# Kernel optimization log

Hardware: AMD Instinct MI355X
Metric: run time of the kernel (lower is better)

## Reference

```python
import jax, jax.numpy as jnp
import numpy as np

B, S, C = 16, 4096, 512
T_MAX = 512          # static max target length (padded, masked)
BETA = 1.0
CIF_EPS = 1e-4
LN_EPS = 1e-5
EXTRA_STEPS = 2      # max number of extra full fires per timestep (alpha<=1 after scaling => rarely >0)


def setup_inputs() -> dict:
    key = jax.random.key(0)
    ks = jax.random.split(key, 5)
    return {
        "x": jax.random.normal(ks[0], (B, S, C), jnp.float32),
        "encoder_padding_mask": jnp.zeros((B, S), bool),
        "target_lengths": jax.random.randint(ks[1], (B,), 1, T_MAX + 1),
        "conv_w": jax.random.normal(ks[2], (C, C, 3), jnp.float32) * 0.02,  # (out,in,k) torch layout
        "conv_b": jnp.zeros((C,), jnp.float32),
        "ln_g": jnp.ones((C,), jnp.float32),
        "ln_b": jnp.zeros((C,), jnp.float32),
        "proj_w": jax.random.normal(ks[3], (C, 1), jnp.float32) * (1.0 / np.sqrt(C)),
        "proj_b": jnp.zeros((1,), jnp.float32),
    }


def weight_predictor(x, conv_w, conv_b, ln_g, ln_b, proj_w, proj_b):
    # x: (B,S,C) -> alpha: (B,S) in (0,1). Dropout is eval-mode identity.
    h = jnp.transpose(x, (0, 2, 1))  # (B,C,S)
    h = jax.lax.conv_general_dilated(
        h, conv_w, window_strides=(1,), padding='SAME',
        dimension_numbers=('NCH', 'OIH', 'NCH')) + conv_b[None, :, None]
    h = jnp.transpose(h, (0, 2, 1))  # (B,S,C)
    mu = jnp.mean(h, -1, keepdims=True)
    var = jnp.mean((h - mu) ** 2, -1, keepdims=True)
    h = (h - mu) * jax.lax.rsqrt(var + LN_EPS) * ln_g + ln_b
    h = jax.nn.gelu(h, approximate=False)
    return jax.nn.sigmoid(h @ proj_w + proj_b)[..., 0]  # (B,S)


def cif(x, alpha, target_lengths):
    # torch-cif parallel formulation (training branch with target_lengths scaling)
    Bb, Ss, Cc = x.shape
    alpha_sum = jnp.sum(alpha, 1)                                   # (B,)
    desired = BETA * target_lengths.astype(alpha.dtype) + CIF_EPS
    alpha = alpha * (desired / alpha_sum)[:, None]
    csum = jnp.cumsum(alpha, 1)                                     # (B,S)
    right_idx = jnp.minimum(jnp.floor(csum / BETA).astype(jnp.int32), T_MAX)
    left_idx = jnp.concatenate(
        [jnp.zeros((Bb, 1), jnp.int32), right_idx[:, :-1]], axis=1)
    fire_num = right_idx - left_idx
    extra = jnp.maximum(fire_num - 1, 0)
    right_w = jnp.where(fire_num > 0, csum - right_idx.astype(alpha.dtype) * BETA, 0.0)
    left_w = alpha - right_w - extra.astype(alpha.dtype) * BETA

    bidx = jnp.arange(Bb)[:, None]  # (B,1) broadcast over S
    out = jnp.zeros((Bb, T_MAX + 1, Cc), x.dtype)
    out = out.at[bidx, left_idx].add(left_w[..., None] * x)
    out = out.at[bidx, right_idx].add(right_w[..., None] * x)
    # extra full-beta fires for steps whose alpha crosses multiple thresholds
    tgt = left_idx
    ew = extra
    for _ in range(EXTRA_STEPS):
        tgt = jnp.minimum(tgt + 1, T_MAX)
        m = (ew > 0).astype(x.dtype)
        out = out.at[bidx, tgt].add((BETA * m)[..., None] * x)
        ew = ew - 1
    out = out[:, :T_MAX]
    valid = (jnp.arange(T_MAX)[None, :] < target_lengths[:, None])  # (B,T)
    return out * valid[..., None]


def reference(x, encoder_padding_mask, target_lengths,
              conv_w, conv_b, ln_g, ln_b, proj_w, proj_b):
    # weight_predictor_stop_gradient=True: detach x for alpha
    alpha = weight_predictor(jax.lax.stop_gradient(x),
                             conv_w, conv_b, ln_g, ln_b, proj_w, proj_b)
    pad = encoder_padding_mask
    x = jnp.where(pad[..., None], 0.0, x)
    alpha = jnp.where(pad, 0.0, alpha)
    return cif(x, alpha, target_lengths)  # (B, T_MAX, C)
```

## Files before the change

### kernel.cpp

```cpp
#include <hip/hip_runtime.h>
#include <math.h>

#define B_DIM 16
#define S_LEN 4096
#define C_DIM 512
#define TMAXI 512

typedef __attribute__((ext_vector_type(8))) short bfrag;
typedef __attribute__((ext_vector_type(4))) float facc;

__device__ __forceinline__ unsigned short f2bf(float f) {
  unsigned u = __float_as_uint(f);
  unsigned r = u + 0x7FFFu + ((u >> 16) & 1u);
  return (unsigned short)(r >> 16);
}
__device__ __forceinline__ float bf2f(unsigned short h) {
  return __uint_as_float(((unsigned)h) << 16);
}

__device__ __forceinline__ void gload16(const void* g, void* l) {
  __builtin_amdgcn_global_load_lds(
      (const __attribute__((address_space(1))) unsigned int*)g,
      (__attribute__((address_space(3))) unsigned int*)l, 16, 0, 0);
}

__device__ __forceinline__ float wave_reduce_add(float v) {
#pragma unroll
  for (int off = 32; off > 0; off >>= 1) v += __shfl_xor(v, off, 64);
  return v;
}

__global__ __launch_bounds__(256) void k_split_x(const float* __restrict__ x,
                                                 unsigned short* __restrict__ xph,
                                                 unsigned short* __restrict__ xpl) {
  const size_t total = (size_t)B_DIM * (S_LEN + 2) * C_DIM;
  size_t e0 = ((size_t)blockIdx.x * 256 + threadIdx.x) * 8;
  if (e0 >= total) return;
  int b = (int)(e0 / ((size_t)(S_LEN + 2) * C_DIM));
  size_t r = e0 - (size_t)b * (S_LEN + 2) * C_DIM;
  int sp = (int)(r / C_DIM);
  int c = (int)(r % C_DIM);
  unsigned short hv[8], lv[8];
  if (sp == 0 || sp == S_LEN + 1) {
#pragma unroll
    for (int j = 0; j < 8; ++j) { hv[j] = 0; lv[j] = 0; }
  } else {
    const float* xs = &x[((size_t)b * S_LEN + (sp - 1)) * C_DIM + c];
    float4 v0 = *(const float4*)xs;
    float4 v1 = *(const float4*)(xs + 4);
    float vv[8] = {v0.x, v0.y, v0.z, v0.w, v1.x, v1.y, v1.z, v1.w};
#pragma unroll
    for (int j = 0; j < 8; ++j) {
      unsigned short h = f2bf(vv[j]);
      hv[j] = h;
      lv[j] = f2bf(vv[j] - bf2f(h));
    }
  }
  *(uint4*)&xph[e0] = *(const uint4*)hv;
  *(uint4*)&xpl[e0] = *(const uint4*)lv;
}

__global__ __launch_bounds__(256) void k_split_w(const float* __restrict__ w,
                                                 unsigned short* __restrict__ wh,
                                                 unsigned short* __restrict__ wl) {
  int idx = blockIdx.x * 256 + threadIdx.x;
  if (idx >= C_DIM * C_DIM) return;
  const float* src = &w[(size_t)idx * 3];
#pragma unroll
  for (int dk = 0; dk < 3; ++dk) {
    float v = src[dk];
    unsigned short h = f2bf(v);
    wh[(size_t)dk * (C_DIM * C_DIM) + idx] = h;
    wl[(size_t)dk * (C_DIM * C_DIM) + idx] = f2bf(v - bf2f(h));
  }
}

__global__ __launch_bounds__(512) void k_fused(const unsigned short* __restrict__ xph,
                                               const unsigned short* __restrict__ xpl,
                                               const unsigned short* __restrict__ wh,
                                               const unsigned short* __restrict__ wl,
                                               const float* __restrict__ conv_b,
                                               const float* __restrict__ ln_g,
                                               const float* __restrict__ ln_b,
                                               const float* __restrict__ pw,
                                               const float* __restrict__ pb,
                                               const unsigned char* __restrict__ mask,
                                               float* __restrict__ alpha) {
  __shared__ short At[64 * 64];
  __shared__ short Bt[512 * 64];

  const int t = threadIdx.x;
  const int lane = t & 63;
  const int wid = t >> 6;
  const int wr = wid >> 2;
  const int wc = wid & 3;
  const int lr = lane & 15;
  const int kg = lane >> 4;

  const int m0 = blockIdx.x * 64;
  const int b = m0 >> 12;
  const int s0 = m0 & (S_LEN - 1);

  const int arow = t >> 3;
  const int aps = t & 7;
  const int als = aps ^ (arow & 7);
  const unsigned short* asrc_base =
      (als < 4 ? xph : xpl) + ((size_t)b * (S_LEN + 2) + (s0 + arow)) * C_DIM + (als & 3) * 8;

  const unsigned short* bsrc_base[8];
#pragma unroll
  for (int r = 0; r < 8; ++r) {
    int c = r * 512 + t;
    int row = c >> 3;
    int ls = (c & 7) ^ (row & 7);
    bsrc_base[r] = (ls < 4 ? wh : wl) + (size_t)row * C_DIM + (ls & 3) * 8;
  }

  facc acc[2][8];
#pragma unroll
  for (int fm = 0; fm < 2; ++fm)
#pragma unroll
    for (int fn = 0; fn < 8; ++fn) acc[fm][fn] = (facc)0.f;

  for (int q = 0; q < 48; ++q) {
    const int dk = q >> 4;
    const int ci0 = (q & 15) << 5;
    __syncthreads();
    gload16(asrc_base + dk * C_DIM + ci0, &At[t * 8]);
    const size_t boff = (size_t)dk * (C_DIM * C_DIM) + ci0;
#pragma unroll
    for (int r = 0; r < 8; ++r) gload16(bsrc_base[r] + boff, &Bt[(r * 512 + t) * 8]);
    __syncthreads();

    bfrag ah[2], al[2];
#pragma unroll
    for (int fm = 0; fm < 2; ++fm) {
      int row = wr * 32 + fm * 16 + lr;
      int ph = kg ^ (row & 7);
      int pl = (4 + kg) ^ (row & 7);
      ah[fm] = *(const bfrag*)&At[row * 64 + ph * 8];
      al[fm] = *(const bfrag*)&At[row * 64 + pl * 8];
    }
#pragma unroll
    for (int fn = 0; fn < 8; ++fn) {
      int col = wc * 128 + fn * 16 + lr;
      int ph = kg ^ (col & 7);
      int pl = (4 + kg) ^ (col & 7);
      bfrag bh = *(const bfrag*)&Bt[col * 64 + ph * 8];
      bfrag bl = *(const bfrag*)&Bt[col * 64 + pl * 8];
#pragma unroll
      for (int fm = 0; fm < 2; ++fm) {
        acc[fm][fn] = __builtin_amdgcn_mfma_f32_16x16x32_bf16(ah[fm], bh, acc[fm][fn], 0, 0, 0);
        acc[fm][fn] = __builtin_amdgcn_mfma_f32_16x16x32_bf16(al[fm], bh, acc[fm][fn], 0, 0, 0);
        acc[fm][fn] = __builtin_amdgcn_mfma_f32_16x16x32_bf16(ah[fm], bl, acc[fm][fn], 0, 0, 0);
      }
    }
  }

  __syncthreads();
  float* red = (float*)At;
  float* mrow = (float*)At + 256;
  float* srow = (float*)At + 320;

  float cb8[8], g8[8], be8[8], w8[8];
#pragma unroll
  for (int fn = 0; fn < 8; ++fn) {
    int col = wc * 128 + fn * 16 + lr;
    cb8[fn] = conv_b[col];
    g8[fn] = ln_g[col];
    be8[fn] = ln_b[col];
    w8[fn] = pw[col];
  }
#pragma unroll
  for (int fm = 0; fm < 2; ++fm)
#pragma unroll
    for (int fn = 0; fn < 8; ++fn)
#pragma unroll
      for (int j = 0; j < 4; ++j) acc[fm][fn][j] += cb8[fn];

#pragma unroll
  for (int fm = 0; fm < 2; ++fm)
#pragma unroll
    for (int j = 0; j < 4; ++j) {
      float s = 0.f;
#pragma unroll
      for (int fn = 0; fn < 8; ++fn) s += acc[fm][fn][j];
      s += __shfl_xor(s, 1, 64); s += __shfl_xor(s, 2, 64);
      s += __shfl_xor(s, 4, 64); s += __shfl_xor(s, 8, 64);
      if (lr == 0) red[(wr * 32 + fm * 16 + kg * 4 + j) * 4 + wc] = s;
    }
  __syncthreads();
  if (t < 64) mrow[t] = (red[t * 4] + red[t * 4 + 1] + red[t * 4 + 2] + red[t * 4 + 3]) * (1.f / 512.f);
  __syncthreads();
  float mu[2][4];
#pragma unroll
  for (int fm = 0; fm < 2; ++fm)
#pragma unroll
    for (int j = 0; j < 4; ++j) mu[fm][j] = mrow[wr * 32 + fm * 16 + kg * 4 + j];

#pragma unroll
  for (int fm = 0; fm < 2; ++fm)
#pragma unroll
    for (int j = 0; j < 4; ++j) {
      float s = 0.f;
#pragma unroll
      for (int fn = 0; fn < 8; ++fn) {
        float d = acc[fm][fn][j] - mu[fm][j];
        s += d * d;
      }
      s += __shfl_xor(s, 1, 64); s += __shfl_xor(s, 2, 64);
      s += __shfl_xor(s, 4, 64); s += __shfl_xor(s, 8, 64);
      if (lr == 0) red[(wr * 32 + fm * 16 + kg * 4 + j) * 4 + wc] = s;
    }
  __syncthreads();
  if (t < 64) srow[t] = 1.0f / sqrtf((red[t * 4] + red[t * 4 + 1] + red[t * 4 + 2] + red[t * 4 + 3]) * (1.f / 512.f) + 1e-5f);
  __syncthreads();
  float rs[2][4];
#pragma unroll
  for (int fm = 0; fm < 2; ++fm)
#pragma unroll
    for (int j = 0; j < 4; ++j) rs[fm][j] = srow[wr * 32 + fm * 16 + kg * 4 + j];

#pragma unroll
  for (int fm = 0; fm < 2; ++fm)
#pragma unroll
    for (int j = 0; j < 4; ++j) {
      float s = 0.f;
#pragma unroll
      for (int fn = 0; fn < 8; ++fn) {
        float y = (acc[fm][fn][j] - mu[fm][j]) * rs[fm][j] * g8[fn] + be8[fn];
        float gel = 0.5f * y * (1.0f + erff(y * 0.70710678118654752440f));
        s += gel * w8[fn];
      }
      s += __shfl_xor(s, 1, 64); s += __shfl_xor(s, 2, 64);
      s += __shfl_xor(s, 4, 64); s += __shfl_xor(s, 8, 64);
      if (lr == 0) red[(wr * 32 + fm * 16 + kg * 4 + j) * 4 + wc] = s;
    }
  __syncthreads();
  if (t < 64) {
    float z = red[t * 4] + red[t * 4 + 1] + red[t * 4 + 2] + red[t * 4 + 3] + pb[0];
    float a = 1.f / (1.f + expf(-z));
    int pos = m0 + t;
    if (mask[pos]) a = 0.f;
    alpha[pos] = a;
  }
}

__global__ __launch_bounds__(256) void k_asum(const float* __restrict__ alpha, float* __restrict__ asum) {
  __shared__ float red[256];
  const int b = blockIdx.x;
  const int t = threadIdx.x;
  float s = 0.f;
  for (int i = t; i < S_LEN; i += 256) s += alpha[(size_t)b * S_LEN + i];
  red[t] = s;
  __syncthreads();
  for (int k = 128; k > 0; k >>= 1) {
    if (t < k) red[t] += red[t + k];
    __syncthreads();
  }
  if (t == 0) asum[b] = red[0];
}

__global__ __launch_bounds__(256) void k_scan(const float* __restrict__ alpha,
                                              const float* __restrict__ asum,
                                              const int* __restrict__ tlen,
                                              float* __restrict__ alphaS,
                                              float* __restrict__ csum,
                                              int* __restrict__ ridx) {
  __shared__ float buf[B_DIM][257];
  __shared__ float cbuf[B_DIM][257];
  __shared__ int ibuf[B_DIM][257];
  __shared__ float run[B_DIM];
  __shared__ float scl[B_DIM];
  const int t = threadIdx.x;
  if (t < B_DIM) {
    run[t] = 0.f;
    float desired = 1.0f * (float)tlen[t] + 1e-4f;
    scl[t] = desired / asum[t];
  }
  __syncthreads();
  for (int c = 0; c < 16; ++c) {
#pragma unroll
    for (int r = 0; r < B_DIM; ++r)
      buf[r][t] = alpha[(size_t)r * S_LEN + c * 256 + t];
    __syncthreads();
    if (t < B_DIM) {
      float r = run[t];
      const float sc = scl[t];
      for (int ss = 0; ss < 256; ++ss) {
        float a = buf[t][ss] * sc;
        r += a;
        buf[t][ss] = a;
        cbuf[t][ss] = r;
        int ri = (int)floorf(r);
        ibuf[t][ss] = ri > TMAXI ? TMAXI : ri;
      }
      run[t] = r;
    }
    __syncthreads();
#pragma unroll
    for (int r = 0; r < B_DIM; ++r) {
      size_t g = (size_t)r * S_LEN + c * 256 + t;
      alphaS[g] = buf[r][t];
      csum[g] = cbuf[r][t];
      ridx[g] = ibuf[r][t];
    }
    __syncthreads();
  }
}

__device__ __forceinline__ int lower_bound(const int* __restrict__ R, int v) {
  int lo = 0, hi = S_LEN;
  while (lo < hi) {
    int m = (lo + hi) >> 1;
    if (R[m] < v) lo = m + 1; else hi = m;
  }
  return lo;
}

__global__ __launch_bounds__(128) void k_out(const float* __restrict__ x,
                                             const float* __restrict__ alphaS,
                                             const float* __restrict__ csum,
                                             const int* __restrict__ ridx,
                                             const int* __restrict__ tlen,
                                             float* __restrict__ out) {
  const int b = blockIdx.y;
  const int tt = blockIdx.x;
  const int c4 = threadIdx.x;
  float4 acc = {0.f, 0.f, 0.f, 0.f};

  if (tt < tlen[b]) {
    const int* R = ridx + (size_t)b * S_LEN;
    const float* aS = alphaS + (size_t)b * S_LEN;
    const float* cS = csum + (size_t)b * S_LEN;
    int lo = lower_bound(R, tt);
    int hi = lower_bound(R, tt + 1);
    if (hi > S_LEN - 1) hi = S_LEN - 1;
    const float* xb = x + ((size_t)b * S_LEN) * C_DIM + c4 * 4;
    for (int s = lo; s <= hi; ++s) {
      int Rs = R[s];
      int Ls = (s > 0) ? R[s - 1] : 0;
      int fire = Rs - Ls;
      float a = aS[s];
      float cs = cS[s];
      float rw = (fire > 0) ? (cs - (float)Rs) : 0.f;
      int extra = (fire > 1) ? (fire - 1) : 0;
      float lw = a - rw - (float)extra;
      float wgt = 0.f;
      if (Ls == tt) wgt += lw;
      if (fire > 0 && Rs == tt) wgt += rw;
      int t1 = (Ls + 1 < TMAXI) ? (Ls + 1) : TMAXI;
      int t2 = (t1 + 1 < TMAXI) ? (t1 + 1) : TMAXI;
      if (extra >= 1 && t1 == tt) wgt += 1.0f;
      if (extra >= 2 && t2 == tt) wgt += 1.0f;
      if (wgt != 0.f) {
        const float4 xv = *(const float4*)&xb[(size_t)s * C_DIM];
        acc.x = fmaf(wgt, xv.x, acc.x);
        acc.y = fmaf(wgt, xv.y, acc.y);
        acc.z = fmaf(wgt, xv.z, acc.z);
        acc.w = fmaf(wgt, xv.w, acc.w);
      }
    }
  }
  *(float4*)&out[(((size_t)b * TMAXI) + tt) * C_DIM + c4 * 4] = acc;
}

extern "C" void kernel_launch(void* const* d_in, const int* in_sizes, int n_in,
                              void* d_out, int out_size, void* d_ws, size_t ws_size,
                              hipStream_t stream) {
  const float* x = (const float*)d_in[0];
  const unsigned char* mask = (const unsigned char*)d_in[1];
  const int* tlen = (const int*)d_in[2];
  const float* conv_w = (const float*)d_in[3];
  const float* conv_b = (const float*)d_in[4];
  const float* ln_g = (const float*)d_in[5];
  const float* ln_b = (const float*)d_in[6];
  const float* proj_w = (const float*)d_in[7];
  const float* proj_b = (const float*)d_in[8];
  float* out = (float*)d_out;

  char* ws = (char*)d_ws;
  const size_t n_pos = (size_t)B_DIM * S_LEN;
  const size_t xp_elems = (size_t)B_DIM * (S_LEN + 2) * C_DIM;

  unsigned short* xph = (unsigned short*)ws;
  unsigned short* xpl = xph + xp_elems;
  unsigned short* wh = xpl + xp_elems;
  unsigned short* wl = wh + (size_t)3 * C_DIM * C_DIM;
  char* p = (char*)(wl + (size_t)3 * C_DIM * C_DIM);
  float* alpha = (float*)p;   p += n_pos * 4;
  float* alphaS = (float*)p;  p += n_pos * 4;
  float* csumb = (float*)p;   p += n_pos * 4;
  int* ridx = (int*)p;        p += n_pos * 4;
  float* asum = (float*)p;

  k_split_w<<<(C_DIM * C_DIM + 255) / 256, 256, 0, stream>>>(conv_w, wh, wl);
  k_split_x<<<(int)((xp_elems / 8 + 255) / 256), 256, 0, stream>>>(x, xph, xpl);
  k_fused<<<(B_DIM * S_LEN) / 64, 512, 0, stream>>>(xph, xpl, wh, wl, conv_b, ln_g, ln_b,
                                                    proj_w, proj_b, mask, alpha);
  k_asum<<<B_DIM, 256, 0, stream>>>(alpha, asum);
  k_scan<<<1, 256, 0, stream>>>(alpha, asum, tlen, alphaS, csumb, ridx);
  k_out<<<dim3(TMAXI, B_DIM), 128, 0, stream>>>(x, alphaS, csumb, ridx, tlen, out);
}
```

Measured before the change: 1.169 ms.

## Enlarge conv GEMM M-tile to 128 and replace gather output with atomic scatter

```diff
diff --git a/kernel.cpp b/kernel.cpp
--- a/kernel.cpp
+++ b/kernel.cpp
@@ -22,12 +22,6 @@
   __builtin_amdgcn_global_load_lds(
       (const __attribute__((address_space(1))) unsigned int*)g,
       (__attribute__((address_space(3))) unsigned int*)l, 16, 0, 0);
-}
-
-__device__ __forceinline__ float wave_reduce_add(float v) {
-#pragma unroll
-  for (int off = 32; off > 0; off >>= 1) v += __shfl_xor(v, off, 64);
-  return v;
 }
 
 __global__ __launch_bounds__(256) void k_split_x(const float* __restrict__ x,
@@ -75,18 +69,18 @@
   }
 }
 
-__global__ __launch_bounds__(512) void k_fused(const unsigned short* __restrict__ xph,
-                                               const unsigned short* __restrict__ xpl,
-                                               const unsigned short* __restrict__ wh,
-                                               const unsigned short* __restrict__ wl,
-                                               const float* __restrict__ conv_b,
-                                               const float* __restrict__ ln_g,
-                                               const float* __restrict__ ln_b,
-                                               const float* __restrict__ pw,
-                                               const float* __restrict__ pb,
-                                               const unsigned char* __restrict__ mask,
-                                               float* __restrict__ alpha) {
-  __shared__ short At[64 * 64];
+__global__ __launch_bounds__(512, 2) void k_fused(const unsigned short* __restrict__ xph,
+                                                  const unsigned short* __restrict__ xpl,
+                                                  const unsigned short* __restrict__ wh,
+                                                  const unsigned short* __restrict__ wl,
+                                                  const float* __restrict__ conv_b,
+                                                  const float* __restrict__ ln_g,
+                                                  const float* __restrict__ ln_b,
+                                                  const float* __restrict__ pw,
+                                                  const float* __restrict__ pb,
+                                                  const unsigned char* __restrict__ mask,
+                                                  float* __restrict__ alpha) {
+  __shared__ short At[128 * 64];
   __shared__ short Bt[512 * 64];
 
   const int t = threadIdx.x;
@@ -97,16 +91,18 @@
   const int lr = lane & 15;
   const int kg = lane >> 4;
 
-  const int m0 = blockIdx.x * 64;
+  const int m0 = blockIdx.x * 128;
   const int b = m0 >> 12;
   const int s0 = m0 & (S_LEN - 1);
 
-  const int arow = t >> 3;
-  const int aps = t & 7;
-  const int als = aps ^ (arow & 7);
-  const unsigned short* asrc_base =
-      (als < 4 ? xph : xpl) + ((size_t)b * (S_LEN + 2) + (s0 + arow)) * C_DIM + (als & 3) * 8;
-
+  const unsigned short* asrc_base[2];
+#pragma unroll
+  for (int r = 0; r < 2; ++r) {
+    int c = r * 512 + t;
+    int row = c >> 3;
+    int ls = (c & 7) ^ (row & 7);
+    asrc_base[r] = (ls < 4 ? xph : xpl) + ((size_t)b * (S_LEN + 2) + (s0 + row)) * C_DIM + (ls & 3) * 8;
+  }
   const unsigned short* bsrc_base[8];
 #pragma unroll
   for (int r = 0; r < 8; ++r) {
@@ -116,9 +112,9 @@
     bsrc_base[r] = (ls < 4 ? wh : wl) + (size_t)row * C_DIM + (ls & 3) * 8;
   }
 
-  facc acc[2][8];
-#pragma unroll
-  for (int fm = 0; fm < 2; ++fm)
+  facc acc[4][8];
+#pragma unroll
+  for (int fm = 0; fm < 4; ++fm)
 #pragma unroll
     for (int fn = 0; fn < 8; ++fn) acc[fm][fn] = (facc)0.f;
 
@@ -126,16 +122,17 @@
     const int dk = q >> 4;
     const int ci0 = (q & 15) << 5;
     __syncthreads();
-    gload16(asrc_base + dk * C_DIM + ci0, &At[t * 8]);
+#pragma unroll
+    for (int r = 0; r < 2; ++r) gload16(asrc_base[r] + dk * C_DIM + ci0, &At[(r * 512 + t) * 8]);
     const size_t boff = (size_t)dk * (C_DIM * C_DIM) + ci0;
 #pragma unroll
     for (int r = 0; r < 8; ++r) gload16(bsrc_base[r] + boff, &Bt[(r * 512 + t) * 8]);
     __syncthreads();
 
-    bfrag ah[2], al[2];
-#pragma unroll
-    for (int fm = 0; fm < 2; ++fm) {
-      int row = wr * 32 + fm * 16 + lr;
+    bfrag ah[4], al[4];
+#pragma unroll
+    for (int fm = 0; fm < 4; ++fm) {
+      int row = wr * 64 + fm * 16 + lr;
       int ph = kg ^ (row & 7);
       int pl = (4 + kg) ^ (row & 7);
       ah[fm] = *(const bfrag*)&At[row * 64 + ph * 8];
@@ -149,7 +146,7 @@
       bfrag bh = *(const bfrag*)&Bt[col * 64 + ph * 8];
       bfrag bl = *(const bfrag*)&Bt[col * 64 + pl * 8];
 #pragma unroll
-      for (int fm = 0; fm < 2; ++fm) {
+      for (int fm = 0; fm < 4; ++fm) {
         acc[fm][fn] = __builtin_amdgcn_mfma_f32_16x16x32_bf16(ah[fm], bh, acc[fm][fn], 0, 0, 0);
         acc[fm][fn] = __builtin_amdgcn_mfma_f32_16x16x32_bf16(al[fm], bh, acc[fm][fn], 0, 0, 0);
         acc[fm][fn] = __builtin_amdgcn_mfma_f32_16x16x32_bf16(ah[fm], bl, acc[fm][fn], 0, 0, 0);
@@ -159,8 +156,8 @@
 
   __syncthreads();
   float* red = (float*)At;
-  float* mrow = (float*)At + 256;
-  float* srow = (float*)At + 320;
+  float* mrow = (float*)At + 512;
+  float* srow = (float*)At + 640;
 
   float cb8[8], g8[8], be8[8], w8[8];
 #pragma unroll
@@ -172,14 +169,14 @@
     w8[fn] = pw[col];
   }
 #pragma unroll
-  for (int fm = 0; fm < 2; ++fm)
+  for (int fm = 0; fm < 4; ++fm)
 #pragma unroll
     for (int fn = 0; fn < 8; ++fn)
 #pragma unroll
       for (int j = 0; j < 4; ++j) acc[fm][fn][j] += cb8[fn];
 
 #pragma unroll
-  for (int fm = 0; fm < 2; ++fm)
+  for (int fm = 0; fm < 4; ++fm)
 #pragma unroll
     for (int j = 0; j < 4; ++j) {
       float s = 0.f;
@@ -187,19 +184,19 @@
       for (int fn = 0; fn < 8; ++fn) s += acc[fm][fn][j];
       s += __shfl_xor(s, 1, 64); s += __shfl_xor(s, 2, 64);
       s += __shfl_xor(s, 4, 64); s += __shfl_xor(s, 8, 64);
-      if (lr == 0) red[(wr * 32 + fm * 16 + kg * 4 + j) * 4 + wc] = s;
-    }
-  __syncthreads();
-  if (t < 64) mrow[t] = (red[t * 4] + red[t * 4 + 1] + red[t * 4 + 2] + red[t * 4 + 3]) * (1.f / 512.f);
-  __syncthreads();
-  float mu[2][4];
-#pragma unroll
-  for (int fm = 0; fm < 2; ++fm)
-#pragma unroll
-    for (int j = 0; j < 4; ++j) mu[fm][j] = mrow[wr * 32 + fm * 16 + kg * 4 + j];
-
-#pragma unroll
-  for (int fm = 0; fm < 2; ++fm)
+      if (lr == 0) red[(wr * 64 + fm * 16 + kg * 4 + j) * 4 + wc] = s;
+    }
+  __syncthreads();
+  if (t < 128) mrow[t] = (red[t * 4] + red[t * 4 + 1] + red[t * 4 + 2] + red[t * 4 + 3]) * (1.f / 512.f);
+  __syncthreads();
+  float mu[4][4];
+#pragma unroll
+  for (int fm = 0; fm < 4; ++fm)
+#pragma unroll
+    for (int j = 0; j < 4; ++j) mu[fm][j] = mrow[wr * 64 + fm * 16 + kg * 4 + j];
+
+#pragma unroll
+  for (int fm = 0; fm < 4; ++fm)
 #pragma unroll
     for (int j = 0; j < 4; ++j) {
       float s = 0.f;
@@ -210,19 +207,19 @@
       }
       s += __shfl_xor(s, 1, 64); s += __shfl_xor(s, 2, 64);
       s += __shfl_xor(s, 4, 64); s += __shfl_xor(s, 8, 64);
-      if (lr == 0) red[(wr * 32 + fm * 16 + kg * 4 + j) * 4 + wc] = s;
-    }
-  __syncthreads();
-  if (t < 64) srow[t] = 1.0f / sqrtf((red[t * 4] + red[t * 4 + 1] + red[t * 4 + 2] + red[t * 4 + 3]) * (1.f / 512.f) + 1e-5f);
-  __syncthreads();
-  float rs[2][4];
-#pragma unroll
-  for (int fm = 0; fm < 2; ++fm)
-#pragma unroll
-    for (int j = 0; j < 4; ++j) rs[fm][j] = srow[wr * 32 + fm * 16 + kg * 4 + j];
-
-#pragma unroll
-  for (int fm = 0; fm < 2; ++fm)
+      if (lr == 0) red[(wr * 64 + fm * 16 + kg * 4 + j) * 4 + wc] = s;
+    }
+  __syncthreads();
+  if (t < 128) srow[t] = 1.0f / sqrtf((red[t * 4] + red[t * 4 + 1] + red[t * 4 + 2] + red[t * 4 + 3]) * (1.f / 512.f) + 1e-5f);
+  __syncthreads();
+  float rs[4][4];
+#pragma unroll
+  for (int fm = 0; fm < 4; ++fm)
+#pragma unroll
+    for (int j = 0; j < 4; ++j) rs[fm][j] = srow[wr * 64 + fm * 16 + kg * 4 + j];
+
+#pragma unroll
+  for (int fm = 0; fm < 4; ++fm)
 #pragma unroll
     for (int j = 0; j < 4; ++j) {
       float s = 0.f;
@@ -234,10 +231,10 @@
       }
       s += __shfl_xor(s, 1, 64); s += __shfl_xor(s, 2, 64);
       s += __shfl_xor(s, 4, 64); s += __shfl_xor(s, 8, 64);
-      if (lr == 0) red[(wr * 32 + fm * 16 + kg * 4 + j) * 4 + wc] = s;
-    }
-  __syncthreads();
-  if (t < 64) {
+      if (lr == 0) red[(wr * 64 + fm * 16 + kg * 4 + j) * 4 + wc] = s;
+    }
+  __syncthreads();
+  if (t < 128) {
     float z = red[t * 4] + red[t * 4 + 1] + red[t * 4 + 2] + red[t * 4 + 3] + pb[0];
     float a = 1.f / (1.f + expf(-z));
     int pos = m0 + t;
@@ -309,60 +306,55 @@
   }
 }
 
-__device__ __forceinline__ int lower_bound(const int* __restrict__ R, int v) {
-  int lo = 0, hi = S_LEN;
-  while (lo < hi) {
-    int m = (lo + hi) >> 1;
-    if (R[m] < v) lo = m + 1; else hi = m;
-  }
-  return lo;
-}
-
-__global__ __launch_bounds__(128) void k_out(const float* __restrict__ x,
-                                             const float* __restrict__ alphaS,
-                                             const float* __restrict__ csum,
-                                             const int* __restrict__ ridx,
-                                             const int* __restrict__ tlen,
-                                             float* __restrict__ out) {
-  const int b = blockIdx.y;
-  const int tt = blockIdx.x;
-  const int c4 = threadIdx.x;
-  float4 acc = {0.f, 0.f, 0.f, 0.f};
-
-  if (tt < tlen[b]) {
-    const int* R = ridx + (size_t)b * S_LEN;
-    const float* aS = alphaS + (size_t)b * S_LEN;
-    const float* cS = csum + (size_t)b * S_LEN;
-    int lo = lower_bound(R, tt);
-    int hi = lower_bound(R, tt + 1);
-    if (hi > S_LEN - 1) hi = S_LEN - 1;
-    const float* xb = x + ((size_t)b * S_LEN) * C_DIM + c4 * 4;
-    for (int s = lo; s <= hi; ++s) {
-      int Rs = R[s];
-      int Ls = (s > 0) ? R[s - 1] : 0;
-      int fire = Rs - Ls;
-      float a = aS[s];
-      float cs = cS[s];
-      float rw = (fire > 0) ? (cs - (float)Rs) : 0.f;
-      int extra = (fire > 1) ? (fire - 1) : 0;
-      float lw = a - rw - (float)extra;
-      float wgt = 0.f;
-      if (Ls == tt) wgt += lw;
-      if (fire > 0 && Rs == tt) wgt += rw;
-      int t1 = (Ls + 1 < TMAXI) ? (Ls + 1) : TMAXI;
-      int t2 = (t1 + 1 < TMAXI) ? (t1 + 1) : TMAXI;
-      if (extra >= 1 && t1 == tt) wgt += 1.0f;
-      if (extra >= 2 && t2 == tt) wgt += 1.0f;
-      if (wgt != 0.f) {
-        const float4 xv = *(const float4*)&xb[(size_t)s * C_DIM];
-        acc.x = fmaf(wgt, xv.x, acc.x);
-        acc.y = fmaf(wgt, xv.y, acc.y);
-        acc.z = fmaf(wgt, xv.z, acc.z);
-        acc.w = fmaf(wgt, xv.w, acc.w);
-      }
-    }
-  }
-  *(float4*)&out[(((size_t)b * TMAXI) + tt) * C_DIM + c4 * 4] = acc;
+__global__ __launch_bounds__(256) void k_scatter(const float* __restrict__ x,
+                                                 const float* __restrict__ alphaS,
+                                                 const float* __restrict__ csum,
+                                                 const int* __restrict__ ridx,
+                                                 const int* __restrict__ tlen,
+                                                 float* __restrict__ out) {
+  const int w = threadIdx.x >> 6;
+  const int lane = threadIdx.x & 63;
+  const int p = blockIdx.x * 4 + w;
+  const int b = p >> 12;
+  const int s = p & (S_LEN - 1);
+
+  const int Rs = ridx[p];
+  const int Ls = (s > 0) ? ridx[p - 1] : 0;
+  const float a = alphaS[p];
+  const float cs = csum[p];
+  const int fire = Rs - Ls;
+  const float rw = (fire > 0) ? (cs - (float)Rs) : 0.f;
+  const int extra = (fire > 1) ? (fire - 1) : 0;
+  const float lw = a - rw - (float)extra;
+  const int tl = tlen[b];
+  const int t1 = (Ls + 1 < TMAXI) ? (Ls + 1) : TMAXI;
+  const int t2 = (t1 + 1 < TMAXI) ? (t1 + 1) : TMAXI;
+
+  int rows[4];
+  float wg[4];
+  int n = 0;
+  if (Ls < tl && lw != 0.f) { rows[n] = Ls; wg[n] = lw; ++n; }
+  if (fire > 0 && Rs < tl && rw != 0.f) { rows[n] = Rs; wg[n] = rw; ++n; }
+  if (extra >= 1 && t1 < tl) { rows[n] = t1; wg[n] = 1.0f; ++n; }
+  if (extra >= 2 && t2 < tl) { rows[n] = t2; wg[n] = 1.0f; ++n; }
+  if (n == 0) return;
+
+  const float* xr = x + ((size_t)b * S_LEN + s) * C_DIM + lane * 8;
+  float4 v0 = *(const float4*)xr;
+  float4 v1 = *(const float4*)(xr + 4);
+
+  for (int i = 0; i < n; ++i) {
+    float* o = out + (((size_t)b * TMAXI) + rows[i]) * C_DIM + lane * 8;
+    const float g = wg[i];
+    unsafeAtomicAdd(&o[0], g * v0.x);
+    unsafeAtomicAdd(&o[1], g * v0.y);
+    unsafeAtomicAdd(&o[2], g * v0.z);
+    unsafeAtomicAdd(&o[3], g * v0.w);
+    unsafeAtomicAdd(&o[4], g * v1.x);
+    unsafeAtomicAdd(&o[5], g * v1.y);
+    unsafeAtomicAdd(&o[6], g * v1.z);
+    unsafeAtomicAdd(&o[7], g * v1.w);
+  }
 }
 
 extern "C" void kernel_launch(void* const* d_in, const int* in_sizes, int n_in,
@@ -394,11 +386,12 @@
   int* ridx = (int*)p;        p += n_pos * 4;
   float* asum = (float*)p;
 
+  hipMemsetAsync(d_out, 0, (size_t)out_size * sizeof(float), stream);
   k_split_w<<<(C_DIM * C_DIM + 255) / 256, 256, 0, stream>>>(conv_w, wh, wl);
   k_split_x<<<(int)((xp_elems / 8 + 255) / 256), 256, 0, stream>>>(x, xph, xpl);
-  k_fused<<<(B_DIM * S_LEN) / 64, 512, 0, stream>>>(xph, xpl, wh, wl, conv_b, ln_g, ln_b,
-                                                    proj_w, proj_b, mask, alpha);
+  k_fused<<<(B_DIM * S_LEN) / 128, 512, 0, stream>>>(xph, xpl, wh, wl, conv_b, ln_g, ln_b,
+                                                     proj_w, proj_b, mask, alpha);
   k_asum<<<B_DIM, 256, 0, stream>>>(alpha, asum);
   k_scan<<<1, 256, 0, stream>>>(alpha, asum, tlen, alphaS, csumb, ridx);
-  k_out<<<dim3(TMAXI, B_DIM), 128, 0, stream>>>(x, alphaS, csumb, ridx, tlen, out);
-}
+  k_scatter<<<(B_DIM * S_LEN) / 4, 256, 0, stream>>>(x, alphaS, csumb, ridx, tlen, out);
+}
```

Result: slower. 1.805 ms (+54.5%).
